# Kernel optimization log

Hardware: AMD Instinct MI355X
Metric: run time of the kernel (lower is better)

## Reference

```python
import jax, jax.numpy as jnp
import numpy as np

N, HW, L = 16, 3136, 64
C_IN, C_OUT, D = 256, 512, 256


def setup_inputs() -> dict:
    key = jax.random.key(0)
    ks = jax.random.split(key, 8)
    # xavier-normal-ish scale for weights
    def xav(k, shape):
        fan_in, fan_out = shape[1], shape[0]
        std = (2.0 / (fan_in + fan_out)) ** 0.5
        return jax.random.normal(k, shape, dtype=jnp.float32) * std
    return {
        "x": jax.random.normal(ks[0], (N, HW, C_IN), dtype=jnp.float32),
        "t": jax.random.normal(ks[1], (N, L, D), dtype=jnp.float32),
        "W1": xav(ks[2], (D, C_IN)),      # linear1 weight (out,in), no bias
        "W2": xav(ks[3], (D, D)),         # linear2 weight, no bias
        "W3": xav(ks[4], (C_OUT, D)),     # linear3 weight
        "b3": jnp.zeros((C_OUT,), dtype=jnp.float32),
        "Wd": xav(ks[5], (C_OUT, C_IN)),  # downsample weight
        "bd": jnp.zeros((C_OUT,), dtype=jnp.float32),
    }


def reference(x, t, W1, W2, W3, b3, Wd, bd):
    # x: (N, HW, C_in), t: (N, L, D)
    x_q = jnp.einsum("npc,dc->npd", x, W1)          # (N, HW, D)
    t_q = jnp.einsum("nld,ed->nle", t, W2)          # (N, L, D)
    a = jnp.einsum("npd,nld->npl", x_q, t_q)        # unscaled QK^T (N, HW, L)
    a = jax.nn.softmax(a, axis=2)
    t3 = jnp.einsum("nld,od->nlo", t, W3) + b3      # (N, L, C_out)
    av = jnp.einsum("npl,nlo->npo", a, t3)          # (N, HW, C_out)
    x_ds = jnp.einsum("npc,oc->npo", x, Wd) + bd    # downsample residual
    return x_ds + av
```

## Files before the change

### kernel.cpp

```cpp
#include <hip/hip_runtime.h>


typedef unsigned short u16;
using half8 = __attribute__((ext_vector_type(8))) _Float16;
using f32x4 = __attribute__((ext_vector_type(4))) float;

__device__ __forceinline__ u16 f2h(float f) {
  _Float16 h = (_Float16)f;
  union { _Float16 h; u16 u; } cv; cv.h = h;
  return cv.u;
}

__device__ __forceinline__ f32x4 mfma16(half8 a, half8 b, f32x4 c) {
  return __builtin_amdgcn_mfma_f32_16x16x32_f16(a, b, c, 0, 0, 0);
}

__global__ __launch_bounds__(256) void prep_kernel(
    const float* __restrict__ W1, const float* __restrict__ W2,
    const float* __restrict__ W3, const float* __restrict__ Wd,
    const float* __restrict__ t,
    u16* __restrict__ W3f, u16* __restrict__ Wdf, u16* __restrict__ tf,
    u16* __restrict__ Gtf) {
  int b = blockIdx.x, k = threadIdx.x;
  if (b < 2048) {
    const float* src; u16* dst; int row;
    if (b < 512)       { src = W3; dst = W3f; row = b; }
    else if (b < 1024) { src = Wd; dst = Wdf; row = b - 512; }
    else               { src = t;  dst = tf;  row = b - 1024; }
    float v = src[(size_t)row*256 + k];
    int flat = ((row >> 4)*8 + (k >> 5))*512 + ((k >> 3) & 3)*128 + (row & 15)*8 + (k & 7);
    dst[flat] = f2h(v);
  } else {
    int c = b - 2048;
    float g = 0.f;
    #pragma unroll 16
    for (int d = 0; d < 256; ++d)
      g = fmaf(W1[d*256 + c], W2[d*256 + k], g);
    int flat = ((c >> 4)*8 + (k >> 5))*512 + ((k >> 3) & 3)*128 + (c & 15)*8 + (k & 7);
    Gtf[flat] = f2h(g);
  }
}

__global__ __launch_bounds__(256) void mt_t3_kernel(
    const u16* __restrict__ tf, const u16* __restrict__ Gtf,
    const u16* __restrict__ W3f, const float* __restrict__ b3,
    u16* __restrict__ mtf, u16* __restrict__ t3f) {
  const int tid = threadIdx.x, w = tid >> 6, lane = tid & 63;
  const int quad = lane >> 4, l16 = lane & 15;
  const int b = blockIdx.x;

  if (b < 64) {
    const int n = b >> 2, eb = b & 3;
    const int gc = eb*4 + w;
    f32x4 acc[4];
    #pragma unroll
    for (int mt = 0; mt < 4; ++mt) acc[mt] = (f32x4){0.f, 0.f, 0.f, 0.f};
    #pragma unroll
    for (int kc = 0; kc < 8; ++kc) {
      half8 bf = *(const half8*)(Gtf + (gc*8 + kc)*512 + lane*8);
      #pragma unroll
      for (int mt = 0; mt < 4; ++mt) {
        half8 a = *(const half8*)(tf + ((n*4 + mt)*8 + kc)*512 + lane*8);
        acc[mt] = mfma16(a, bf, acc[mt]);
      }
    }
    #pragma unroll
    for (int mt = 0; mt < 4; ++mt)
      #pragma unroll
      for (int r = 0; r < 4; ++r) {
        int flat = ((n*4 + mt)*8 + eb*2 + (w >> 1))*512
                 + ((w & 1)*2 + (l16 >> 3))*128 + (quad*4 + r)*8 + (l16 & 7);
        mtf[flat] = f2h(acc[mt][r]);
      }
  } else {
    const int b2 = b - 64;
    const int n = b2 >> 3, ob = b2 & 7;
    const int gW3 = ob*4 + w;
    f32x4 acc[4];
    #pragma unroll
    for (int nt = 0; nt < 4; ++nt) acc[nt] = (f32x4){0.f, 0.f, 0.f, 0.f};
    #pragma unroll
    for (int kc = 0; kc < 8; ++kc) {
      half8 a = *(const half8*)(W3f + (gW3*8 + kc)*512 + lane*8);
      #pragma unroll
      for (int nt = 0; nt < 4; ++nt) {
        half8 bf = *(const half8*)(tf + ((n*4 + nt)*8 + kc)*512 + lane*8);
        acc[nt] = mfma16(a, bf, acc[nt]);
      }
    }
    #pragma unroll
    for (int nt = 0; nt < 4; ++nt)
      #pragma unroll
      for (int r = 0; r < 4; ++r) {
        int o = ob*64 + w*16 + quad*4 + r;
        int flat = ((n*32 + ob*4 + w)*2 + (nt >> 1))*512
                 + ((nt & 1)*2 + (l16 >> 3))*128 + (quad*4 + r)*8 + (l16 & 7);
        t3f[flat] = f2h(acc[nt][r] + b3[o]);
      }
  }
}

__global__ __launch_bounds__(512, 4) void main_kernel(
    const float* __restrict__ x, const u16* __restrict__ Wdf,
    const u16* __restrict__ mtf, const u16* __restrict__ t3f,
    const float* __restrict__ bd, float* __restrict__ out) {
  __shared__ __attribute__((aligned(16))) char smem[44032];
  u16* xs = (u16*)smem;
  u16* aw = (u16*)(smem + 33792);
  float* parts = (float*)(smem + 43008);

  const int bid = blockIdx.x;
  const int n  = bid / 49;
  const int pt = bid - n*49;
  const int m0 = pt * 64;
  const int tid = threadIdx.x, w = tid >> 6, lane = tid & 63;
  const int quad = lane >> 4, l16 = lane & 15;
  const int rg = w & 3;
  const int lp = w >> 2;

  float4 bias4[4];
  #pragma unroll
  for (int ot = 0; ot < 4; ++ot)
    bias4[ot] = *(const float4*)&bd[w*64 + ot*16 + quad*4];

  {
    const float4* xg = (const float4*)(x + (size_t)(n*3136 + m0)*256);
    #pragma unroll
    for (int it = 0; it < 8; ++it) {
      int idx = it*512 + tid;
      int r = idx >> 6, c4 = idx & 63;
      float4 v = xg[idx];
      ushort4 u;
      u.x = f2h(v.x); u.y = f2h(v.y); u.z = f2h(v.z); u.w = f2h(v.w);
      *(ushort4*)(&xs[r*264 + c4*4]) = u;
    }
  }
  __syncthreads();

  f32x4 acc2[2];
  acc2[0] = (f32x4){0.f, 0.f, 0.f, 0.f};
  acc2[1] = (f32x4){0.f, 0.f, 0.f, 0.f};
  #pragma unroll
  for (int kc = 0; kc < 8; ++kc) {
    half8 a = *(const half8*)(&xs[(rg*16 + l16)*264 + kc*32 + quad*8]);
    #pragma unroll
    for (int j = 0; j < 2; ++j) {
      half8 bf = *(const half8*)(mtf + ((size_t)(n*4 + lp*2 + j)*8 + kc)*512 + lane*8);
      acc2[j] = mfma16(a, bf, acc2[j]);
    }
  }

  float mx_[4], ps_[4], e0_[4], e1_[4];
  #pragma unroll
  for (int r = 0; r < 4; ++r) {
    float s0 = acc2[0][r], s1 = acc2[1][r];
    float mx = fmaxf(s0, s1);
    #pragma unroll
    for (int off = 8; off >= 1; off >>= 1) mx = fmaxf(mx, __shfl_xor(mx, off, 64));
    float e0 = __expf(s0 - mx), e1 = __expf(s1 - mx);
    float ps = e0 + e1;
    #pragma unroll
    for (int off = 8; off >= 1; off >>= 1) ps += __shfl_xor(ps, off, 64);
    mx_[r] = mx; ps_[r] = ps; e0_[r] = e0; e1_[r] = e1;
    if (l16 == 0) {
      int row = rg*16 + quad*4 + r;
      parts[(row*2 + lp)*2]     = mx;
      parts[(row*2 + lp)*2 + 1] = ps;
    }
  }
  __syncthreads();

  #pragma unroll
  for (int r = 0; r < 4; ++r) {
    int row = rg*16 + quad*4 + r;
    float mxo = parts[(row*2 + (1 - lp))*2];
    float pso = parts[(row*2 + (1 - lp))*2 + 1];
    float g  = fmaxf(mx_[r], mxo);
    float sA = __expf(mx_[r] - g), sB = __expf(mxo - g);
    float inv = 1.0f / (ps_[r]*sA + pso*sB);
    float scl = sA * inv;
    aw[row*72 + (lp*2)*16 + l16]     = f2h(e0_[r]*scl);
    aw[row*72 + (lp*2 + 1)*16 + l16] = f2h(e1_[r]*scl);
  }
  __syncthreads();

  f32x4 acc[4][4];
  #pragma unroll
  for (int ot = 0; ot < 4; ++ot)
    #pragma unroll
    for (int ptt = 0; ptt < 4; ++ptt) acc[ot][ptt] = (f32x4){0.f, 0.f, 0.f, 0.f};
  #pragma unroll
  for (int kc = 0; kc < 8; ++kc) {
    half8 bx[4];
    #pragma unroll
    for (int ptt = 0; ptt < 4; ++ptt)
      bx[ptt] = *(const half8*)(&xs[(ptt*16 + l16)*264 + kc*32 + quad*8]);
    #pragma unroll
    for (int ot = 0; ot < 4; ++ot) {
      half8 af = *(const half8*)(Wdf + ((size_t)(w*4 + ot)*8 + kc)*512 + lane*8);
      #pragma unroll
      for (int ptt = 0; ptt < 4; ++ptt) acc[ot][ptt] = mfma16(af, bx[ptt], acc[ot][ptt]);
    }
  }
  #pragma unroll
  for (int kc3 = 0; kc3 < 2; ++kc3) {
    half8 ba[4];
    #pragma unroll
    for (int ptt = 0; ptt < 4; ++ptt)
      ba[ptt] = *(const half8*)(&aw[(ptt*16 + l16)*72 + kc3*32 + quad*8]);
    #pragma unroll
    for (int ot = 0; ot < 4; ++ot) {
      half8 af = *(const half8*)(t3f + ((size_t)(n*32 + w*4 + ot)*2 + kc3)*512 + lane*8);
      #pragma unroll
      for (int ptt = 0; ptt < 4; ++ptt) acc[ot][ptt] = mfma16(af, ba[ptt], acc[ot][ptt]);
    }
  }

  #pragma unroll
  for (int ptt = 0; ptt < 4; ++ptt) {
    float* orow = out + (size_t)(n*3136 + m0 + ptt*16 + l16)*512 + w*64 + quad*4;
    #pragma unroll
    for (int ot = 0; ot < 4; ++ot) {
      float4 v;
      v.x = acc[ot][ptt][0] + bias4[ot].x;
      v.y = acc[ot][ptt][1] + bias4[ot].y;
      v.z = acc[ot][ptt][2] + bias4[ot].z;
      v.w = acc[ot][ptt][3] + bias4[ot].w;
      *(float4*)(orow + ot*16) = v;
    }
  }
}

extern "C" void kernel_launch(void* const* d_in, const int* in_sizes, int n_in,
                              void* d_out, int out_size, void* d_ws, size_t ws_size,
                              hipStream_t stream) {
  const float* x  = (const float*)d_in[0];
  const float* t  = (const float*)d_in[1];
  const float* W1 = (const float*)d_in[2];
  const float* W2 = (const float*)d_in[3];
  const float* W3 = (const float*)d_in[4];
  const float* b3 = (const float*)d_in[5];
  const float* Wd = (const float*)d_in[6];
  const float* bd = (const float*)d_in[7];
  float* out = (float*)d_out;

  char* ws = (char*)d_ws;
  u16* W3f = (u16*)(ws + 0);
  u16* Wdf = (u16*)(ws + 262144);
  u16* tf  = (u16*)(ws + 524288);
  u16* Gtf = (u16*)(ws + 1048576);
  u16* mtf = (u16*)(ws + 1179648);
  u16* t3f = (u16*)(ws + 1703936);

  hipLaunchKernelGGL(prep_kernel, dim3(2304), dim3(256), 0, stream,
                     W1, W2, W3, Wd, t, W3f, Wdf, tf, Gtf);
  hipLaunchKernelGGL(mt_t3_kernel, dim3(192), dim3(256), 0, stream,
                     tf, Gtf, W3f, b3, mtf, t3f);
  hipLaunchKernelGGL(main_kernel, dim3(784), dim3(512), 0, stream,
                     x, Wdf, mtf, t3f, bd, out);
}
```

Before: 221.5 us.

## Reassociate query projection, defer sync, stage output stores through LDS

```diff
diff --git a/kernel.cpp b/kernel.cpp
--- a/kernel.cpp
+++ b/kernel.cpp
@@ -19,61 +19,78 @@
     const float* __restrict__ W1, const float* __restrict__ W2,
     const float* __restrict__ W3, const float* __restrict__ Wd,
     const float* __restrict__ t,
-    u16* __restrict__ W3f, u16* __restrict__ Wdf, u16* __restrict__ tf,
-    u16* __restrict__ Gtf) {
+    u16* __restrict__ W1Tf, u16* __restrict__ W2f, u16* __restrict__ W3f,
+    u16* __restrict__ Wdf, u16* __restrict__ tf) {
   int b = blockIdx.x, k = threadIdx.x;
-  if (b < 2048) {
-    const float* src; u16* dst; int row;
-    if (b < 512)       { src = W3; dst = W3f; row = b; }
-    else if (b < 1024) { src = Wd; dst = Wdf; row = b - 512; }
-    else               { src = t;  dst = tf;  row = b - 1024; }
-    float v = src[(size_t)row*256 + k];
-    int flat = ((row >> 4)*8 + (k >> 5))*512 + ((k >> 3) & 3)*128 + (row & 15)*8 + (k & 7);
-    dst[flat] = f2h(v);
-  } else {
-    int c = b - 2048;
-    float g = 0.f;
-    #pragma unroll 16
-    for (int d = 0; d < 256; ++d)
-      g = fmaf(W1[d*256 + c], W2[d*256 + k], g);
-    int flat = ((c >> 4)*8 + (k >> 5))*512 + ((k >> 3) & 3)*128 + (c & 15)*8 + (k & 7);
-    Gtf[flat] = f2h(g);
-  }
+  float v; u16* dst; int row;
+  if (b < 256)       { dst = W1Tf; row = b;        v = W1[(size_t)k*256 + b]; }
+  else if (b < 512)  { dst = W2f;  row = b - 256;  v = W2[(size_t)row*256 + k]; }
+  else if (b < 1024) { dst = W3f;  row = b - 512;  v = W3[(size_t)row*256 + k]; }
+  else if (b < 1536) { dst = Wdf;  row = b - 1024; v = Wd[(size_t)row*256 + k]; }
+  else               { dst = tf;   row = b - 1536; v = t[(size_t)row*256 + k]; }
+  int flat = ((row >> 4)*8 + (k >> 5))*512 + ((k >> 3) & 3)*128 + (row & 15)*8 + (k & 7);
+  dst[flat] = f2h(v);
 }
 
 __global__ __launch_bounds__(256) void mt_t3_kernel(
-    const u16* __restrict__ tf, const u16* __restrict__ Gtf,
-    const u16* __restrict__ W3f, const float* __restrict__ b3,
+    const u16* __restrict__ tf, const u16* __restrict__ W1Tf,
+    const u16* __restrict__ W2f, const u16* __restrict__ W3f,
+    const float* __restrict__ b3,
     u16* __restrict__ mtf, u16* __restrict__ t3f) {
+  __shared__ u16 tqs[16384];
   const int tid = threadIdx.x, w = tid >> 6, lane = tid & 63;
   const int quad = lane >> 4, l16 = lane & 15;
   const int b = blockIdx.x;
 
-  if (b < 64) {
-    const int n = b >> 2, eb = b & 3;
-    const int gc = eb*4 + w;
-    f32x4 acc[4];
-    #pragma unroll
-    for (int mt = 0; mt < 4; ++mt) acc[mt] = (f32x4){0.f, 0.f, 0.f, 0.f};
-    #pragma unroll
-    for (int kc = 0; kc < 8; ++kc) {
-      half8 bf = *(const half8*)(Gtf + (gc*8 + kc)*512 + lane*8);
-      #pragma unroll
-      for (int mt = 0; mt < 4; ++mt) {
-        half8 a = *(const half8*)(tf + ((n*4 + mt)*8 + kc)*512 + lane*8);
-        acc[mt] = mfma16(a, bf, acc[mt]);
-      }
-    }
-    #pragma unroll
-    for (int mt = 0; mt < 4; ++mt)
-      #pragma unroll
-      for (int r = 0; r < 4; ++r) {
-        int flat = ((n*4 + mt)*8 + eb*2 + (w >> 1))*512
-                 + ((w & 1)*2 + (l16 >> 3))*128 + (quad*4 + r)*8 + (l16 & 7);
-        mtf[flat] = f2h(acc[mt][r]);
-      }
+  if (b < 16) {
+    const int n = b;
+    #pragma unroll
+    for (int q = 0; q < 4; ++q) {
+      const int g = q*4 + w;
+      f32x4 acc[4];
+      #pragma unroll
+      for (int mt = 0; mt < 4; ++mt) acc[mt] = (f32x4){0.f, 0.f, 0.f, 0.f};
+      #pragma unroll
+      for (int kc = 0; kc < 8; ++kc) {
+        half8 bf = *(const half8*)(W2f + (g*8 + kc)*512 + lane*8);
+        #pragma unroll
+        for (int mt = 0; mt < 4; ++mt) {
+          half8 a = *(const half8*)(tf + ((n*4 + mt)*8 + kc)*512 + lane*8);
+          acc[mt] = mfma16(a, bf, acc[mt]);
+        }
+      }
+      #pragma unroll
+      for (int mt = 0; mt < 4; ++mt)
+        #pragma unroll
+        for (int r = 0; r < 4; ++r)
+          tqs[(mt*8 + (g >> 1))*512 + ((g & 1)*2 + (l16 >> 3))*128
+              + (quad*4 + r)*8 + (l16 & 7)] = f2h(acc[mt][r]);
+    }
+    __syncthreads();
+    #pragma unroll
+    for (int q = 0; q < 4; ++q) {
+      const int gc = q*4 + w;
+      f32x4 acc[4];
+      #pragma unroll
+      for (int mt = 0; mt < 4; ++mt) acc[mt] = (f32x4){0.f, 0.f, 0.f, 0.f};
+      #pragma unroll
+      for (int kc = 0; kc < 8; ++kc) {
+        half8 bf = *(const half8*)(W1Tf + (gc*8 + kc)*512 + lane*8);
+        #pragma unroll
+        for (int mt = 0; mt < 4; ++mt) {
+          half8 a = *(const half8*)(&tqs[(mt*8 + kc)*512 + lane*8]);
+          acc[mt] = mfma16(a, bf, acc[mt]);
+        }
+      }
+      #pragma unroll
+      for (int mt = 0; mt < 4; ++mt)
+        #pragma unroll
+        for (int r = 0; r < 4; ++r)
+          mtf[((n*4 + mt)*8 + (gc >> 1))*512 + ((gc & 1)*2 + (l16 >> 3))*128
+              + (quad*4 + r)*8 + (l16 & 7)] = f2h(acc[mt][r]);
+    }
   } else {
-    const int b2 = b - 64;
+    const int b2 = b - 16;
     const int n = b2 >> 3, ob = b2 & 7;
     const int gW3 = ob*4 + w;
     f32x4 acc[4];
@@ -104,10 +121,11 @@
     const float* __restrict__ x, const u16* __restrict__ Wdf,
     const u16* __restrict__ mtf, const u16* __restrict__ t3f,
     const float* __restrict__ bd, float* __restrict__ out) {
-  __shared__ __attribute__((aligned(16))) char smem[44032];
+  __shared__ __attribute__((aligned(16))) char smem[78848];
   u16* xs = (u16*)smem;
   u16* aw = (u16*)(smem + 33792);
   float* parts = (float*)(smem + 43008);
+  float* scb = (float*)(smem + 44032);
 
   const int bid = blockIdx.x;
   const int n  = bid / 49;
@@ -118,10 +136,10 @@
   const int rg = w & 3;
   const int lp = w >> 2;
 
-  float4 bias4[4];
+  f32x4 bias4[4];
   #pragma unroll
   for (int ot = 0; ot < 4; ++ot)
-    bias4[ot] = *(const float4*)&bd[w*64 + ot*16 + quad*4];
+    bias4[ot] = *(const f32x4*)&bd[w*64 + ot*16 + quad*4];
 
   {
     const float4* xg = (const float4*)(x + (size_t)(n*3136 + m0)*256);
@@ -182,7 +200,6 @@
     aw[row*72 + (lp*2)*16 + l16]     = f2h(e0_[r]*scl);
     aw[row*72 + (lp*2 + 1)*16 + l16] = f2h(e1_[r]*scl);
   }
-  __syncthreads();
 
   f32x4 acc[4][4];
   #pragma unroll
@@ -202,6 +219,8 @@
       for (int ptt = 0; ptt < 4; ++ptt) acc[ot][ptt] = mfma16(af, bx[ptt], acc[ot][ptt]);
     }
   }
+  __syncthreads();
+
   #pragma unroll
   for (int kc3 = 0; kc3 < 2; ++kc3) {
     half8 ba[4];
@@ -216,17 +235,20 @@
     }
   }
 
+  float* sc = scb + w*1088;
   #pragma unroll
   for (int ptt = 0; ptt < 4; ++ptt) {
-    float* orow = out + (size_t)(n*3136 + m0 + ptt*16 + l16)*512 + w*64 + quad*4;
     #pragma unroll
     for (int ot = 0; ot < 4; ++ot) {
-      float4 v;
-      v.x = acc[ot][ptt][0] + bias4[ot].x;
-      v.y = acc[ot][ptt][1] + bias4[ot].y;
-      v.z = acc[ot][ptt][2] + bias4[ot].z;
-      v.w = acc[ot][ptt][3] + bias4[ot].w;
-      *(float4*)(orow + ot*16) = v;
+      f32x4 v = acc[ot][ptt] + bias4[ot];
+      *(f32x4*)&sc[l16*68 + ot*16 + quad*4] = v;
+    }
+    #pragma unroll
+    for (int shot = 0; shot < 4; ++shot) {
+      int row = shot*4 + quad;
+      f32x4 v = *(f32x4*)&sc[row*68 + l16*4];
+      __builtin_nontemporal_store(v,
+        (f32x4*)(out + (size_t)(n*3136 + m0 + ptt*16 + row)*512 + w*64 + l16*4));
     }
   }
 }
@@ -245,17 +267,18 @@
   float* out = (float*)d_out;
 
   char* ws = (char*)d_ws;
-  u16* W3f = (u16*)(ws + 0);
-  u16* Wdf = (u16*)(ws + 262144);
-  u16* tf  = (u16*)(ws + 524288);
-  u16* Gtf = (u16*)(ws + 1048576);
-  u16* mtf = (u16*)(ws + 1179648);
-  u16* t3f = (u16*)(ws + 1703936);
-
-  hipLaunchKernelGGL(prep_kernel, dim3(2304), dim3(256), 0, stream,
-                     W1, W2, W3, Wd, t, W3f, Wdf, tf, Gtf);
-  hipLaunchKernelGGL(mt_t3_kernel, dim3(192), dim3(256), 0, stream,
-                     tf, Gtf, W3f, b3, mtf, t3f);
+  u16* W1Tf = (u16*)(ws + 0);
+  u16* W2f  = (u16*)(ws + 131072);
+  u16* W3f  = (u16*)(ws + 262144);
+  u16* Wdf  = (u16*)(ws + 524288);
+  u16* tf   = (u16*)(ws + 786432);
+  u16* mtf  = (u16*)(ws + 1310720);
+  u16* t3f  = (u16*)(ws + 1835008);
+
+  hipLaunchKernelGGL(prep_kernel, dim3(2560), dim3(256), 0, stream,
+                     W1, W2, W3, Wd, t, W1Tf, W2f, W3f, Wdf, tf);
+  hipLaunchKernelGGL(mt_t3_kernel, dim3(144), dim3(256), 0, stream,
+                     tf, W1Tf, W2f, W3f, b3, mtf, t3f);
   hipLaunchKernelGGL(main_kernel, dim3(784), dim3(512), 0, stream,
                      x, Wdf, mtf, t3f, bd, out);
 }
```

New measurement: 226.9 us. +2.4%, slower.
